# Kernel tuning notes

Measured on AMD Instinct MI355X. Metric: run time of the kernel, lower is better.

The kernel has to match this reference:

```python
import jax, jax.numpy as jnp
import numpy as np

NUM_TOKENS = 2048
HIDDEN = 2048
MOE_INTER = 1408
N_EXPERTS = 16
TOP_K = 4
N_SHARED = 2
SHARED_INTER = N_SHARED * MOE_INTER  # 2816
CAPACITY = 768
ROUTED_SCALE = 1.0


def setup_inputs() -> dict:
    key = jax.random.key(0)
    ks = jax.random.split(key, 9)
    s = 0.02  # init scale for stability
    return {
        "hidden_states": jax.random.normal(ks[0], (NUM_TOKENS, HIDDEN), jnp.float32),
        "w_gate": jax.random.normal(ks[1], (N_EXPERTS, HIDDEN), jnp.float32) * s,
        "w1": jax.random.normal(ks[2], (N_EXPERTS, HIDDEN, MOE_INTER), jnp.float32) * s,  # gate_proj
        "w3": jax.random.normal(ks[3], (N_EXPERTS, HIDDEN, MOE_INTER), jnp.float32) * s,  # up_proj
        "w2": jax.random.normal(ks[4], (N_EXPERTS, MOE_INTER, HIDDEN), jnp.float32) * s,  # down_proj
        "ws1": jax.random.normal(ks[5], (HIDDEN, SHARED_INTER), jnp.float32) * s,
        "ws3": jax.random.normal(ks[6], (HIDDEN, SHARED_INTER), jnp.float32) * s,
        "ws2": jax.random.normal(ks[7], (SHARED_INTER, HIDDEN), jnp.float32) * s,
    }


def _moe_forward(x, w_gate, w1, w3, w2, ws1, ws3, ws2):
    T, d = x.shape
    E = w1.shape[0]
    # ---- router: softmax scores, top-k selection (DeepSeek-V2, norm_topk_prob=False) ----
    scores = jax.nn.softmax(x @ w_gate.T, axis=-1)            # [T, E]
    topw, topi = jax.lax.top_k(scores, TOP_K)                 # [T, K]
    topw = topw * ROUTED_SCALE
    flat_e = topi.reshape(-1)                                 # [T*K] expert id per slot
    flat_w = topw.reshape(-1)                                 # [T*K]
    tok_ids = jnp.repeat(jnp.arange(T), TOP_K)                # [T*K]
    # ---- dispatch: position of each slot within its expert's buffer ----
    onehot = jax.nn.one_hot(flat_e, E, dtype=jnp.int32)       # [T*K, E]
    pos = jnp.take_along_axis(jnp.cumsum(onehot, axis=0), flat_e[:, None], axis=1)[:, 0] - 1
    valid = (pos < CAPACITY).astype(x.dtype)
    buf = jnp.zeros((E, CAPACITY, d), x.dtype).at[flat_e, pos].set(x[tok_ids], mode='drop')
    # ---- grouped SwiGLU expert FFN ----
    g = jnp.einsum('ecd,edi->eci', buf, w1)
    u = jnp.einsum('ecd,edi->eci', buf, w3)
    o = jnp.einsum('eci,eid->ecd', jax.nn.silu(g) * u, w2)    # [E, C, d]
    # ---- combine: gather back, weight, scatter-add per token ----
    gathered = o[flat_e, jnp.clip(pos, 0, CAPACITY - 1)] * (flat_w * valid)[:, None]
    routed = jax.ops.segment_sum(gathered, tok_ids, num_segments=T)  # [T, d]
    # ---- shared experts (always-on SwiGLU) ----
    shared = (jax.nn.silu(x @ ws1) * (x @ ws3)) @ ws2
    return routed + shared


def reference(hidden_states, w_gate, w1, w3, w2, ws1, ws3, ws2):
    return _moe_forward(hidden_states, w_gate, w1, w3, w2, ws1, ws3, ws2)
```

## Files before the change

### kernel.cpp

```cpp
#include <hip/hip_runtime.h>
#include <hip/hip_bf16.h>
#include <cstdint>

#define T_TOKENS 2048
#define HIDDEN 2048
#define INTER 1408
#define NEXP 16
#define TOPK 4
#define SINTER 2816
#define CAP 768
#define BK 32

typedef __attribute__((ext_vector_type(8))) short short8;
typedef __attribute__((ext_vector_type(8))) unsigned short ushort8;
typedef __attribute__((ext_vector_type(4))) float f32x4;

__device__ __forceinline__ float4 ld4f(const float* p) {
  return *reinterpret_cast<const float4*>(p);
}

__device__ __forceinline__ unsigned short f2bf(float v) {
  unsigned int u = __float_as_uint(v);
  unsigned int r = (u + 0x7FFFu + ((u >> 16) & 1u)) >> 16;
  return (unsigned short)r;
}

__device__ __forceinline__ void gld16(const void* g, void* l) {
  __builtin_amdgcn_global_load_lds(
      (const __attribute__((address_space(1))) void*)g,
      (__attribute__((address_space(3))) void*)l, 16, 0, 0);
}

__global__ __launch_bounds__(64) void router_kernel(
    const float* __restrict__ x, const float* __restrict__ wg,
    int* __restrict__ topi, float* __restrict__ topw)
{
  const int t = blockIdx.x;
  const int lane = threadIdx.x;
  float acc[NEXP];
#pragma unroll
  for (int e = 0; e < NEXP; ++e) acc[e] = 0.f;
  const float* xr = x + (size_t)t * HIDDEN;
  for (int i = lane; i < HIDDEN; i += 64) {
    float xv = xr[i];
#pragma unroll
    for (int e = 0; e < NEXP; ++e) acc[e] += xv * wg[e * HIDDEN + i];
  }
#pragma unroll
  for (int e = 0; e < NEXP; ++e) {
#pragma unroll
    for (int off = 32; off > 0; off >>= 1)
      acc[e] += __shfl_xor(acc[e], off);
  }
  float m = acc[0];
#pragma unroll
  for (int e = 1; e < NEXP; ++e) m = fmaxf(m, acc[e]);
  float p[NEXP];
  float s = 0.f;
#pragma unroll
  for (int e = 0; e < NEXP; ++e) { p[e] = expf(acc[e] - m); s += p[e]; }
  const float inv = 1.f / s;
#pragma unroll
  for (int e = 0; e < NEXP; ++e) p[e] *= inv;
  if (lane == 0) {
#pragma unroll
    for (int k = 0; k < TOPK; ++k) {
      float best = -1.f; int bi = 0;
#pragma unroll
      for (int e = 0; e < NEXP; ++e)
        if (p[e] > best) { best = p[e]; bi = e; }
      topi[t * TOPK + k] = bi;
      topw[t * TOPK + k] = best;
      p[bi] = -1.f;
    }
  }
}

__global__ __launch_bounds__(1024) void partition_kernel(
    const int* __restrict__ topi, float* __restrict__ topw,
    int* __restrict__ rowtok, int* __restrict__ count)
{
  __shared__ int se[T_TOKENS * TOPK];
  for (int i = threadIdx.x; i < T_TOKENS * TOPK; i += 1024) se[i] = topi[i];
  __syncthreads();

  const int wave = threadIdx.x >> 6;
  const int lane = threadIdx.x & 63;
  const uint64_t below = (lane == 0) ? 0ull : ((~0ull) >> (64 - lane));
  int base = 0;
  for (int c = 0; c < T_TOKENS * TOPK; c += 64) {
    int ev = se[c + lane];
    uint64_t mask = __ballot(ev == wave);
    if (ev == wave) {
      int my = base + __popcll(mask & below);
      if (my < CAP) rowtok[wave * CAP + my] = c + lane;
      else          topw[c + lane] = 0.f;
    }
    base += __popcll(mask);
  }
  if (lane == 0) count[wave] = base < CAP ? base : CAP;
}

__global__ __launch_bounds__(256) void cvt_x_kernel(
    const float* __restrict__ x, unsigned short* __restrict__ xb)
{
  const long i = ((long)blockIdx.x * 256 + threadIdx.x) * 8;
  float4 a = ld4f(x + i), b = ld4f(x + i + 4);
  float v[8] = {a.x, a.y, a.z, a.w, b.x, b.y, b.z, b.w};
  unsigned short o[8];
#pragma unroll
  for (int j = 0; j < 8; ++j) o[j] = f2bf(v[j]);
  *(ushort8*)(xb + i) = *(ushort8*)&o[0];
}

__global__ __launch_bounds__(256) void tcvt_w_kernel(
    const float* __restrict__ W, unsigned short* __restrict__ T,
    int K, int N)
{
  const long z = blockIdx.z;
  W += z * (long)K * N;
  T += z * (long)K * N;
  const int k0 = blockIdx.x * 64, n0 = blockIdx.y * 64;
  __shared__ float tile[64][65];
  const int tr = threadIdx.x >> 4;
  const int tc4 = (threadIdx.x & 15) * 4;
#pragma unroll
  for (int p = 0; p < 4; ++p) {
    int r = p * 16 + tr;
    float4 v = ld4f(W + (long)(k0 + r) * N + n0 + tc4);
    tile[r][tc4] = v.x; tile[r][tc4 + 1] = v.y;
    tile[r][tc4 + 2] = v.z; tile[r][tc4 + 3] = v.w;
  }
  __syncthreads();
  const int wn = threadIdx.x >> 3;
  const int wk = (threadIdx.x & 7) * 8;
#pragma unroll
  for (int p = 0; p < 2; ++p) {
    int n = p * 32 + wn;
    unsigned short o[8];
#pragma unroll
    for (int j = 0; j < 8; ++j) o[j] = f2bf(tile[wk + j][n]);
    *(ushort8*)(T + (long)(n0 + n) * K + k0 + wk) = *(ushort8*)&o[0];
  }
}

template<int EPI>
__global__ __launch_bounds__(256, 2)
void gemm_bf(const unsigned short* __restrict__ Ag, int ldka,
             const unsigned short* __restrict__ Bg, long bstride,
             float* __restrict__ C, unsigned short* __restrict__ H, int ldc,
             const float* __restrict__ G,
             const int* __restrict__ arows_g, int ashift, long aexp,
             const int* __restrict__ crows_g, long cexp,
             const int* __restrict__ cnt, int Mfix, int K,
             int MT, int NTn)
{
  const int nwg = gridDim.x;
  const int lin = (blockIdx.x & 7) * (nwg >> 3) + (blockIdx.x >> 3);
  const int mt = lin % MT;
  const int rest = lin / MT;
  const int nt = rest % NTn;
  const int e = rest / NTn;

  const int M = cnt ? cnt[e] : Mfix;
  if (mt * 128 >= M) return;
  const int n0 = nt * 128;

  const int tid = threadIdx.x;
  const int l = tid & 63;
  const int w = tid >> 6;
  const int wm = w >> 1;
  const int wn = w & 1;
  const int fr = l & 15;
  const int fc = l >> 4;

  const int* arows = arows_g ? arows_g + e * CAP : nullptr;
  const int* crows = crows_g ? crows_g + e * CAP : nullptr;
  const unsigned short* Bexp = Bg + (long)e * bstride;

  __shared__ __align__(16) unsigned short sA[2][128 * BK];
  __shared__ __align__(16) unsigned short sB[2][128 * BK];

  const int rb_s = ((l >> 3) & 1) | (((l >> 5) & 1) << 1);
  const int sch = ((l & 3) ^ rb_s) * 8;
  long aoff[2], boff[2];
#pragma unroll
  for (int j = 0; j < 2; ++j) {
    const int rloc = j * 64 + w * 16 + (l >> 2);
    int r = mt * 128 + rloc;
    if (r > M - 1) r = M - 1;
    const long arow = arows ? (long)(arows[r] >> ashift) : (aexp * e + r);
    aoff[j] = arow * (long)ldka + sch;
    boff[j] = (long)(n0 + rloc) * K + sch;
  }

  const int rb_r = ((fr >> 1) & 1) | (((fr >> 3) & 1) << 1);
  const int pcoff = (fc ^ rb_r) * 8;

  f32x4 acc[4][4];
#pragma unroll
  for (int i = 0; i < 4; ++i)
#pragma unroll
    for (int j = 0; j < 4; ++j) acc[i][j] = (f32x4)0.f;

  const int NT = K / BK;

  auto stage = [&](int buf, int kt) {
#pragma unroll
    for (int j = 0; j < 2; ++j) {
      gld16(Ag + aoff[j] + kt, &sA[buf][(j * 64 + w * 16) * BK]);
      gld16(Bexp + boff[j] + kt, &sB[buf][(j * 64 + w * 16) * BK]);
    }
  };

  stage(0, 0);
  asm volatile("s_waitcnt vmcnt(0)" ::: "memory");
  __syncthreads();

  for (int t = 0; t < NT; ++t) {
    const int cur = t & 1;
    if (t + 1 < NT) stage(cur ^ 1, (t + 1) * BK);

    short8 fa[4], fb[4];
#pragma unroll
    for (int mi = 0; mi < 4; ++mi)
      fa[mi] = *(const short8*)&sA[cur][(wm * 64 + mi * 16 + fr) * BK + pcoff];
#pragma unroll
    for (int ni = 0; ni < 4; ++ni)
      fb[ni] = *(const short8*)&sB[cur][(wn * 64 + ni * 16 + fr) * BK + pcoff];
#pragma unroll
    for (int mi = 0; mi < 4; ++mi)
#pragma unroll
      for (int ni = 0; ni < 4; ++ni)
        acc[mi][ni] = __builtin_amdgcn_mfma_f32_16x16x32_bf16(fa[mi], fb[ni], acc[mi][ni], 0, 0, 0);

    asm volatile("s_waitcnt vmcnt(0)" ::: "memory");
    __syncthreads();
  }

#pragma unroll
  for (int mi = 0; mi < 4; ++mi)
#pragma unroll
    for (int rr = 0; rr < 4; ++rr) {
      const int r = mt * 128 + wm * 64 + mi * 16 + fc * 4 + rr;
      if (r >= M) continue;
      const long crow = crows ? (long)crows[r] : (cexp * e + r);
#pragma unroll
      for (int ni = 0; ni < 4; ++ni) {
        const int col = n0 + wn * 64 + ni * 16 + fr;
        const long off = crow * (long)ldc + col;
        const float v = acc[mi][ni][rr];
        if constexpr (EPI == 1) {
          const float g = G[off];
          const float h = v * (g / (1.f + __expf(-g)));
          H[off] = f2bf(h);
        } else {
          C[off] = v;
        }
      }
    }
}

__global__ __launch_bounds__(256) void combine_kernel(
    const float* __restrict__ o_slot, const float* __restrict__ topw,
    float* __restrict__ out)
{
  const int t = blockIdx.x;
  float w[TOPK];
#pragma unroll
  for (int k = 0; k < TOPK; ++k) w[k] = topw[t * TOPK + k];
  float* orow = out + (size_t)t * HIDDEN;
  for (int c = threadIdx.x * 4; c < HIDDEN; c += 256 * 4) {
    float4 acc = *reinterpret_cast<float4*>(orow + c);
#pragma unroll
    for (int k = 0; k < TOPK; ++k) {
      if (w[k] != 0.f) {
        float4 v = ld4f(o_slot + ((size_t)(t * TOPK + k)) * HIDDEN + c);
        acc.x += w[k] * v.x; acc.y += w[k] * v.y;
        acc.z += w[k] * v.z; acc.w += w[k] * v.w;
      }
    }
    *reinterpret_cast<float4*>(orow + c) = acc;
  }
}

extern "C" void kernel_launch(void* const* d_in, const int* in_sizes, int n_in,
                              void* d_out, int out_size, void* d_ws, size_t ws_size,
                              hipStream_t stream)
{
  const float* x   = (const float*)d_in[0];
  const float* wg  = (const float*)d_in[1];
  const float* w1  = (const float*)d_in[2];
  const float* w3  = (const float*)d_in[3];
  const float* w2  = (const float*)d_in[4];
  const float* ws1 = (const float*)d_in[5];
  const float* ws3 = (const float*)d_in[6];
  const float* ws2 = (const float*)d_in[7];
  float* out = (float*)d_out;

  char* w = (char*)d_ws;
  int*   topi   = (int*)w;   w += (size_t)T_TOKENS * TOPK * 4;
  float* topw   = (float*)w; w += (size_t)T_TOKENS * TOPK * 4;
  int*   rowtok = (int*)w;   w += (size_t)NEXP * CAP * 4;
  int*   count  = (int*)w;   w += 256;
  uintptr_t a = (uintptr_t)w; a = (a + 255) & ~(uintptr_t)255; w = (char*)a;

  const size_t XSZ  = (size_t)T_TOKENS * HIDDEN;
  const size_t WSSZ = (size_t)HIDDEN * SINTER;
  const size_t WRSZ = (size_t)NEXP * HIDDEN * INTER;
  const size_t HSSZ = (size_t)T_TOKENS * SINTER;
  const size_t HRSZ = (size_t)NEXP * CAP * INTER;

  unsigned short* xb = (unsigned short*)w; w += XSZ * 2;
  unsigned short* wS = (unsigned short*)w; w += WSSZ * 2;
  unsigned short* wR = (unsigned short*)w; w += WRSZ * 2;
  unsigned short* hs = (unsigned short*)w; w += HSSZ * 2;
  unsigned short* hr = (unsigned short*)w; w += HRSZ * 2;
  float* gbuf = (float*)w;   w += (size_t)NEXP * CAP * INTER * 4;
  float* o_slot = gbuf;

  router_kernel<<<T_TOKENS, 64, 0, stream>>>(x, wg, topi, topw);
  partition_kernel<<<1, 1024, 0, stream>>>(topi, topw, rowtok, count);
  cvt_x_kernel<<<(int)(XSZ / (256 * 8)), 256, 0, stream>>>(x, xb);

  tcvt_w_kernel<<<dim3(HIDDEN / 64, SINTER / 64, 1), 256, 0, stream>>>(ws1, wS, HIDDEN, SINTER);
  gemm_bf<0><<<(T_TOKENS / 128) * (SINTER / 128), 256, 0, stream>>>(
      xb, HIDDEN, wS, 0L, gbuf, nullptr, SINTER, nullptr,
      nullptr, 0, 0L, nullptr, 0L,
      nullptr, T_TOKENS, HIDDEN, T_TOKENS / 128, SINTER / 128);
  tcvt_w_kernel<<<dim3(HIDDEN / 64, SINTER / 64, 1), 256, 0, stream>>>(ws3, wS, HIDDEN, SINTER);
  gemm_bf<1><<<(T_TOKENS / 128) * (SINTER / 128), 256, 0, stream>>>(
      xb, HIDDEN, wS, 0L, nullptr, hs, SINTER, gbuf,
      nullptr, 0, 0L, nullptr, 0L,
      nullptr, T_TOKENS, HIDDEN, T_TOKENS / 128, SINTER / 128);

  tcvt_w_kernel<<<dim3(HIDDEN / 64, INTER / 64, NEXP), 256, 0, stream>>>(w1, wR, HIDDEN, INTER);
  gemm_bf<0><<<(CAP / 128) * (INTER / 128) * NEXP, 256, 0, stream>>>(
      xb, HIDDEN, wR, (long)INTER * HIDDEN, gbuf, nullptr, INTER, nullptr,
      rowtok, 2, 0L, nullptr, (long)CAP,
      count, 0, HIDDEN, CAP / 128, INTER / 128);
  tcvt_w_kernel<<<dim3(HIDDEN / 64, INTER / 64, NEXP), 256, 0, stream>>>(w3, wR, HIDDEN, INTER);
  gemm_bf<1><<<(CAP / 128) * (INTER / 128) * NEXP, 256, 0, stream>>>(
      xb, HIDDEN, wR, (long)INTER * HIDDEN, nullptr, hr, INTER, gbuf,
      rowtok, 2, 0L, nullptr, (long)CAP,
      count, 0, HIDDEN, CAP / 128, INTER / 128);

  tcvt_w_kernel<<<dim3(SINTER / 64, HIDDEN / 64, 1), 256, 0, stream>>>(ws2, wS, SINTER, HIDDEN);
  gemm_bf<0><<<(T_TOKENS / 128) * (HIDDEN / 128), 256, 0, stream>>>(
      hs, SINTER, wS, 0L, out, nullptr, HIDDEN, nullptr,
      nullptr, 0, 0L, nullptr, 0L,
      nullptr, T_TOKENS, SINTER, T_TOKENS / 128, HIDDEN / 128);

  tcvt_w_kernel<<<dim3(INTER / 64, HIDDEN / 64, NEXP), 256, 0, stream>>>(w2, wR, INTER, HIDDEN);
  gemm_bf<0><<<(CAP / 128) * (HIDDEN / 128) * NEXP, 256, 0, stream>>>(
      hr, INTER, wR, (long)HIDDEN * INTER, o_slot, nullptr, HIDDEN, nullptr,
      nullptr, 0, (long)CAP, rowtok, 0L,
      count, 0, INTER, CAP / 128, HIDDEN / 128);

  combine_kernel<<<T_TOKENS, 256, 0, stream>>>(o_slot, topw, out);
}
```

Before: 691.6 us.

## Fuse gate/up GEMMs via interleaved weights and triple-buffer GEMM pipeline

Gate and up projection weights are transposed into a 16-row interleaved layout, so one GEMM computes both projections per tile and applies SiLU(g)*u directly in registers. This removes the fp32 intermediate gate buffer write and read-back, and halves the number of GEMM launches that reread the activations. The GEMM main loop also moves from double to triple buffering in LDS with partial vmcnt waits and a single barrier per iteration, so global loads overlap compute more deeply. The cost is 50% more LDS per block, which may limit occupancy under the 2-blocks-per-CU bound.

```diff
diff --git a/kernel.cpp b/kernel.cpp
--- a/kernel.cpp
+++ b/kernel.cpp
@@ -115,11 +115,11 @@
 
 __global__ __launch_bounds__(256) void tcvt_w_kernel(
     const float* __restrict__ W, unsigned short* __restrict__ T,
-    int K, int N)
+    int K, int N, long tz, int mul, int which)
 {
   const long z = blockIdx.z;
   W += z * (long)K * N;
-  T += z * (long)K * N;
+  T += z * tz;
   const int k0 = blockIdx.x * 64, n0 = blockIdx.y * 64;
   __shared__ float tile[64][65];
   const int tr = threadIdx.x >> 4;
@@ -140,7 +140,9 @@
     unsigned short o[8];
 #pragma unroll
     for (int j = 0; j < 8; ++j) o[j] = f2bf(tile[wk + j][n]);
-    *(ushort8*)(T + (long)(n0 + n) * K + k0 + wk) = *(ushort8*)&o[0];
+    const int gn = n0 + n;
+    const long prow = ((long)(gn >> 4) * mul + which) * 16 + (gn & 15);
+    *(ushort8*)(T + prow * K + k0 + wk) = *(ushort8*)&o[0];
   }
 }
 
@@ -149,7 +151,6 @@
 void gemm_bf(const unsigned short* __restrict__ Ag, int ldka,
              const unsigned short* __restrict__ Bg, long bstride,
              float* __restrict__ C, unsigned short* __restrict__ H, int ldc,
-             const float* __restrict__ G,
              const int* __restrict__ arows_g, int ashift, long aexp,
              const int* __restrict__ crows_g, long cexp,
              const int* __restrict__ cnt, int Mfix, int K,
@@ -178,8 +179,8 @@
   const int* crows = crows_g ? crows_g + e * CAP : nullptr;
   const unsigned short* Bexp = Bg + (long)e * bstride;
 
-  __shared__ __align__(16) unsigned short sA[2][128 * BK];
-  __shared__ __align__(16) unsigned short sB[2][128 * BK];
+  __shared__ __align__(16) unsigned short sA[3][128 * BK];
+  __shared__ __align__(16) unsigned short sB[3][128 * BK];
 
   const int rb_s = ((l >> 3) & 1) | (((l >> 5) & 1) << 1);
   const int sch = ((l & 3) ^ rb_s) * 8;
@@ -214,28 +215,32 @@
   };
 
   stage(0, 0);
-  asm volatile("s_waitcnt vmcnt(0)" ::: "memory");
-  __syncthreads();
-
+  stage(1, BK);
+
+  int rb = 0, wb = 2;
   for (int t = 0; t < NT; ++t) {
-    const int cur = t & 1;
-    if (t + 1 < NT) stage(cur ^ 1, (t + 1) * BK);
+    if (t + 1 < NT) asm volatile("s_waitcnt vmcnt(4)" ::: "memory");
+    else            asm volatile("s_waitcnt vmcnt(0)" ::: "memory");
+    __builtin_amdgcn_s_barrier();
+    __builtin_amdgcn_sched_barrier(0);
+
+    if (t + 2 < NT) stage(wb, (t + 2) * BK);
 
     short8 fa[4], fb[4];
 #pragma unroll
     for (int mi = 0; mi < 4; ++mi)
-      fa[mi] = *(const short8*)&sA[cur][(wm * 64 + mi * 16 + fr) * BK + pcoff];
+      fa[mi] = *(const short8*)&sA[rb][(wm * 64 + mi * 16 + fr) * BK + pcoff];
 #pragma unroll
     for (int ni = 0; ni < 4; ++ni)
-      fb[ni] = *(const short8*)&sB[cur][(wn * 64 + ni * 16 + fr) * BK + pcoff];
+      fb[ni] = *(const short8*)&sB[rb][(wn * 64 + ni * 16 + fr) * BK + pcoff];
 #pragma unroll
     for (int mi = 0; mi < 4; ++mi)
 #pragma unroll
       for (int ni = 0; ni < 4; ++ni)
         acc[mi][ni] = __builtin_amdgcn_mfma_f32_16x16x32_bf16(fa[mi], fb[ni], acc[mi][ni], 0, 0, 0);
 
-    asm volatile("s_waitcnt vmcnt(0)" ::: "memory");
-    __syncthreads();
+    rb = (rb == 2) ? 0 : rb + 1;
+    wb = (wb == 2) ? 0 : wb + 1;
   }
 
 #pragma unroll
@@ -245,17 +250,20 @@
       const int r = mt * 128 + wm * 64 + mi * 16 + fc * 4 + rr;
       if (r >= M) continue;
       const long crow = crows ? (long)crows[r] : (cexp * e + r);
-#pragma unroll
-      for (int ni = 0; ni < 4; ++ni) {
-        const int col = n0 + wn * 64 + ni * 16 + fr;
-        const long off = crow * (long)ldc + col;
-        const float v = acc[mi][ni][rr];
-        if constexpr (EPI == 1) {
-          const float g = G[off];
-          const float h = v * (g / (1.f + __expf(-g)));
-          H[off] = f2bf(h);
-        } else {
-          C[off] = v;
+      if constexpr (EPI == 2) {
+#pragma unroll
+        for (int np = 0; np < 2; ++np) {
+          const float g = acc[mi][2 * np][rr];
+          const float u = acc[mi][2 * np + 1][rr];
+          const float h = u * (g / (1.f + __expf(-g)));
+          const int i = (n0 / 32 + 2 * wn + np) * 16 + fr;
+          H[crow * (long)ldc + i] = f2bf(h);
+        }
+      } else {
+#pragma unroll
+        for (int ni = 0; ni < 4; ++ni) {
+          const int col = n0 + wn * 64 + ni * 16 + fr;
+          C[crow * (long)ldc + col] = acc[mi][ni][rr];
         }
       }
     }
@@ -306,54 +314,53 @@
   uintptr_t a = (uintptr_t)w; a = (a + 255) & ~(uintptr_t)255; w = (char*)a;
 
   const size_t XSZ  = (size_t)T_TOKENS * HIDDEN;
-  const size_t WSSZ = (size_t)HIDDEN * SINTER;
-  const size_t WRSZ = (size_t)NEXP * HIDDEN * INTER;
+  const size_t WSI  = (size_t)2 * HIDDEN * SINTER;
+  const size_t WRI  = (size_t)2 * NEXP * HIDDEN * INTER;
   const size_t HSSZ = (size_t)T_TOKENS * SINTER;
   const size_t HRSZ = (size_t)NEXP * CAP * INTER;
 
-  unsigned short* xb = (unsigned short*)w; w += XSZ * 2;
-  unsigned short* wS = (unsigned short*)w; w += WSSZ * 2;
-  unsigned short* wR = (unsigned short*)w; w += WRSZ * 2;
-  unsigned short* hs = (unsigned short*)w; w += HSSZ * 2;
-  unsigned short* hr = (unsigned short*)w; w += HRSZ * 2;
-  float* gbuf = (float*)w;   w += (size_t)NEXP * CAP * INTER * 4;
-  float* o_slot = gbuf;
+  unsigned short* xb  = (unsigned short*)w; w += XSZ * 2;
+  unsigned short* wSi = (unsigned short*)w; w += WSI * 2;
+  unsigned short* wRi = (unsigned short*)w; w += WRI * 2;
+  unsigned short* hs  = (unsigned short*)w; w += HSSZ * 2;
+  unsigned short* hr  = (unsigned short*)w; w += HRSZ * 2;
+  unsigned short* wS2 = wSi;
+  unsigned short* wR2 = wRi;
+  float* o_slot = (float*)(wRi + (size_t)NEXP * HIDDEN * INTER);
 
   router_kernel<<<T_TOKENS, 64, 0, stream>>>(x, wg, topi, topw);
   partition_kernel<<<1, 1024, 0, stream>>>(topi, topw, rowtok, count);
   cvt_x_kernel<<<(int)(XSZ / (256 * 8)), 256, 0, stream>>>(x, xb);
 
-  tcvt_w_kernel<<<dim3(HIDDEN / 64, SINTER / 64, 1), 256, 0, stream>>>(ws1, wS, HIDDEN, SINTER);
-  gemm_bf<0><<<(T_TOKENS / 128) * (SINTER / 128), 256, 0, stream>>>(
-      xb, HIDDEN, wS, 0L, gbuf, nullptr, SINTER, nullptr,
+  tcvt_w_kernel<<<dim3(HIDDEN / 64, SINTER / 64, 1), 256, 0, stream>>>(
+      ws1, wSi, HIDDEN, SINTER, 0L, 2, 0);
+  tcvt_w_kernel<<<dim3(HIDDEN / 64, SINTER / 64, 1), 256, 0, stream>>>(
+      ws3, wSi, HIDDEN, SINTER, 0L, 2, 1);
+  gemm_bf<2><<<(T_TOKENS / 128) * (2 * SINTER / 128), 256, 0, stream>>>(
+      xb, HIDDEN, wSi, 0L, nullptr, hs, SINTER,
       nullptr, 0, 0L, nullptr, 0L,
-      nullptr, T_TOKENS, HIDDEN, T_TOKENS / 128, SINTER / 128);
-  tcvt_w_kernel<<<dim3(HIDDEN / 64, SINTER / 64, 1), 256, 0, stream>>>(ws3, wS, HIDDEN, SINTER);
-  gemm_bf<1><<<(T_TOKENS / 128) * (SINTER / 128), 256, 0, stream>>>(
-      xb, HIDDEN, wS, 0L, nullptr, hs, SINTER, gbuf,
-      nullptr, 0, 0L, nullptr, 0L,
-      nullptr, T_TOKENS, HIDDEN, T_TOKENS / 128, SINTER / 128);
-
-  tcvt_w_kernel<<<dim3(HIDDEN / 64, INTER / 64, NEXP), 256, 0, stream>>>(w1, wR, HIDDEN, INTER);
-  gemm_bf<0><<<(CAP / 128) * (INTER / 128) * NEXP, 256, 0, stream>>>(
-      xb, HIDDEN, wR, (long)INTER * HIDDEN, gbuf, nullptr, INTER, nullptr,
+      nullptr, T_TOKENS, HIDDEN, T_TOKENS / 128, 2 * SINTER / 128);
+
+  tcvt_w_kernel<<<dim3(HIDDEN / 64, INTER / 64, NEXP), 256, 0, stream>>>(
+      w1, wRi, HIDDEN, INTER, (long)2 * HIDDEN * INTER, 2, 0);
+  tcvt_w_kernel<<<dim3(HIDDEN / 64, INTER / 64, NEXP), 256, 0, stream>>>(
+      w3, wRi, HIDDEN, INTER, (long)2 * HIDDEN * INTER, 2, 1);
+  gemm_bf<2><<<(CAP / 128) * (2 * INTER / 128) * NEXP, 256, 0, stream>>>(
+      xb, HIDDEN, wRi, (long)2 * HIDDEN * INTER, nullptr, hr, INTER,
       rowtok, 2, 0L, nullptr, (long)CAP,
-      count, 0, HIDDEN, CAP / 128, INTER / 128);
-  tcvt_w_kernel<<<dim3(HIDDEN / 64, INTER / 64, NEXP), 256, 0, stream>>>(w3, wR, HIDDEN, INTER);
-  gemm_bf<1><<<(CAP / 128) * (INTER / 128) * NEXP, 256, 0, stream>>>(
-      xb, HIDDEN, wR, (long)INTER * HIDDEN, nullptr, hr, INTER, gbuf,
-      rowtok, 2, 0L, nullptr, (long)CAP,
-      count, 0, HIDDEN, CAP / 128, INTER / 128);
-
-  tcvt_w_kernel<<<dim3(SINTER / 64, HIDDEN / 64, 1), 256, 0, stream>>>(ws2, wS, SINTER, HIDDEN);
+      count, 0, HIDDEN, CAP / 128, 2 * INTER / 128);
+
+  tcvt_w_kernel<<<dim3(SINTER / 64, HIDDEN / 64, 1), 256, 0, stream>>>(
+      ws2, wS2, SINTER, HIDDEN, 0L, 1, 0);
   gemm_bf<0><<<(T_TOKENS / 128) * (HIDDEN / 128), 256, 0, stream>>>(
-      hs, SINTER, wS, 0L, out, nullptr, HIDDEN, nullptr,
+      hs, SINTER, wS2, 0L, out, nullptr, HIDDEN,
       nullptr, 0, 0L, nullptr, 0L,
       nullptr, T_TOKENS, SINTER, T_TOKENS / 128, HIDDEN / 128);
 
-  tcvt_w_kernel<<<dim3(INTER / 64, HIDDEN / 64, NEXP), 256, 0, stream>>>(w2, wR, INTER, HIDDEN);
+  tcvt_w_kernel<<<dim3(INTER / 64, HIDDEN / 64, NEXP), 256, 0, stream>>>(
+      w2, wR2, INTER, HIDDEN, (long)INTER * HIDDEN, 1, 0);
   gemm_bf<0><<<(CAP / 128) * (HIDDEN / 128) * NEXP, 256, 0, stream>>>(
-      hr, INTER, wR, (long)HIDDEN * INTER, o_slot, nullptr, HIDDEN, nullptr,
+      hr, INTER, wR2, (long)INTER * HIDDEN, o_slot, nullptr, HIDDEN,
       nullptr, 0, (long)CAP, rowtok, 0L,
       count, 0, INTER, CAP / 128, HIDDEN / 128);
 
```

After: 635.8 us. 1.09x faster.
